# Performance work log

Hardware: AMD Instinct MI355X
Metric: run time of the kernel (lower is better)

## Reference

```python
import jax, jax.numpy as jnp
import numpy as np

N_ATOMS = 100000
N_EDGES = 200000  # paired: edge 2i and 2i+1 are reverses of each other
N_MOLS = 4096
D_V, D_E, D_H = 133, 14, 512
DEPTH = 3
BN_EPS = 1e-5


def setup_inputs() -> dict:
    key = jax.random.key(0)
    ks = jax.random.split(key, 10)
    V = jax.random.normal(ks[0], (N_ATOMS, D_V), dtype=jnp.float32)
    E = jax.random.normal(ks[1], (N_EDGES, D_E), dtype=jnp.float32)
    # paired directed edges: (src,dst) at 2i, (dst,src) at 2i+1 -> rev index is i^1
    half = N_EDGES // 2
    s = jax.random.randint(ks[2], (half,), 0, N_ATOMS, dtype=jnp.int32)
    d = jax.random.randint(ks[3], (half,), 0, N_ATOMS, dtype=jnp.int32)
    edge_src = jnp.stack([s, d], axis=1).reshape(-1)
    edge_dst = jnp.stack([d, s], axis=1).reshape(-1)
    batch = jnp.sort(jax.random.randint(ks[4], (N_ATOMS,), 0, N_MOLS, dtype=jnp.int32))
    sc = 0.02
    W_i = jax.random.normal(ks[5], (D_V + D_E, D_H), dtype=jnp.float32) * sc
    W_h = jax.random.normal(ks[6], (D_H, D_H), dtype=jnp.float32) * sc
    W_o = jax.random.normal(ks[7], (D_V + D_H, D_H), dtype=jnp.float32) * sc
    b_o = jnp.zeros((D_H,), dtype=jnp.float32)
    gamma = jnp.ones((D_H,), dtype=jnp.float32)
    beta = jnp.zeros((D_H,), dtype=jnp.float32)
    return {"V": V, "E": E, "edge_src": edge_src, "edge_dst": edge_dst,
            "batch": batch, "W_i": W_i, "W_h": W_h, "W_o": W_o, "b_o": b_o,
            "gamma": gamma, "beta": beta}


def reference(V, E, edge_src, edge_dst, batch, W_i, W_h, W_o, b_o, gamma, beta):
    n_atoms = V.shape[0]
    n_edges = E.shape[0]
    rev = jnp.arange(n_edges, dtype=jnp.int32) ^ 1  # reverse-bond index

    # --- BondMessagePassing (chemprop v2) ---
    # initialize: H_0 = W_i([V[src] ; E]), H = relu(H_0)
    H0 = jnp.concatenate([V[edge_src], E], axis=1) @ W_i  # [n_edges, d_h]
    H = jax.nn.relu(H0)
    for _ in range(DEPTH - 1):
        # message: sum of incoming edge states at dst node, gathered at src,
        # minus the reverse edge's own state
        M_node = jax.ops.segment_sum(H, edge_dst, num_segments=n_atoms)
        M = M_node[edge_src] - H[rev]
        # update: H = relu(H_0 + W_h(M)) (dropout = 0)
        H = jax.nn.relu(H0 + M @ W_h)
    # finalize: aggregate edges to nodes, H_v = relu(W_o([V ; M_v]))
    M_v = jax.ops.segment_sum(H, edge_dst, num_segments=n_atoms)
    H_v = jax.nn.relu(jnp.concatenate([V, M_v], axis=1) @ W_o + b_o)  # [n_atoms, d_h]

    # --- MeanAggregation over batch ids ---
    sums = jax.ops.segment_sum(H_v, batch, num_segments=N_MOLS)
    counts = jax.ops.segment_sum(jnp.ones((n_atoms,), H_v.dtype), batch, num_segments=N_MOLS)
    h_mol = sums / jnp.maximum(counts, 1.0)[:, None]  # [n_mols, d_h]

    # --- BatchNorm1d (training mode: batch statistics, biased variance) ---
    mu = h_mol.mean(axis=0)
    var = h_mol.var(axis=0)
    return (h_mol - mu) * jax.lax.rsqrt(var + BN_EPS) * gamma + beta
```

## Files before the change

kernel.cpp:

```cpp
#include <hip/hip_runtime.h>

typedef _Float16 f16;
typedef _Float16 half8 __attribute__((ext_vector_type(8)));
typedef _Float16 half4v __attribute__((ext_vector_type(4)));
typedef float f32x4 __attribute__((ext_vector_type(4)));

#define N_ATOMS 100000
#define N_EDGES 200000
#define N_MOLS  4096
#define D_V 133
#define D_E 14
#define D_H 512
#define KC  672
#define KSE 21
#define LDA 40

__global__ void wt_build_swz(const float* __restrict__ W1, int r1,
                             const float* __restrict__ W2, int r2,
                             f16* __restrict__ WtS) {
    int gid = blockIdx.x * blockDim.x + threadIdx.x;
    if (gid >= D_H * KC) return;
    int n = gid / KC;
    int k = gid - n * KC;
    float x = 0.f;
    if (k < r1) x = W1[k * D_H + n];
    else if (k < r1 + r2) x = W2[(k - r1) * D_H + n];
    const int dst = ((((n >> 4) * KSE + (k >> 5)) << 6) + (((k >> 3) & 3) << 4) + (n & 15)) * 8 + (k & 7);
    WtS[dst] = (f16)x;
}

__global__ void csr_hist(const int* __restrict__ edst, int* __restrict__ cnt) {
    int e = blockIdx.x * blockDim.x + threadIdx.x;
    if (e < N_EDGES) atomicAdd(&cnt[edst[e]], 1);
}

__global__ __launch_bounds__(1024) void csr_scan(const int* __restrict__ cnt,
                                                 int* __restrict__ off, int* __restrict__ pos) {
    __shared__ int sums[1024];
    const int tid = threadIdx.x;
    const int lo = tid * 100;
    int s = 0;
    if (lo < N_ATOMS) {
        const int4* c4 = reinterpret_cast<const int4*>(cnt + lo);
        #pragma unroll
        for (int i = 0; i < 25; ++i) { int4 v = c4[i]; s += v.x + v.y + v.z + v.w; }
    }
    sums[tid] = s;
    __syncthreads();
    for (int d = 1; d < 1024; d <<= 1) {
        int v = (tid >= d) ? sums[tid - d] : 0;
        __syncthreads();
        sums[tid] += v;
        __syncthreads();
    }
    int run = sums[tid] - s;
    if (lo < N_ATOMS) {
        const int4* c4 = reinterpret_cast<const int4*>(cnt + lo);
        for (int i = 0; i < 25; ++i) {
            int4 v = c4[i];
            const int b = lo + i * 4;
            off[b]     = run; pos[b]     = run; run += v.x;
            off[b + 1] = run; pos[b + 1] = run; run += v.y;
            off[b + 2] = run; pos[b + 2] = run; run += v.z;
            off[b + 3] = run; pos[b + 3] = run; run += v.w;
        }
    }
    if (tid == 1023) off[N_ATOMS] = run;
}

__global__ void csr_scatter(const int* __restrict__ edst, int* __restrict__ pos,
                            int* __restrict__ eid) {
    int e = blockIdx.x * blockDim.x + threadIdx.x;
    if (e < N_EDGES) {
        int idx = atomicAdd(&pos[edst[e]], 1);
        eid[idx] = e;
    }
}

template<bool F16M>
__global__ __launch_bounds__(512) void seg_csr(
    const f16* __restrict__ H, const int* __restrict__ off, const int* __restrict__ eid,
    void* __restrict__ MnOut, float* __restrict__ Msc)
{
    const int n = blockIdx.x * 8 + (threadIdx.x >> 6);
    const int lane = threadIdx.x & 63;
    const int j0 = off[n], j1 = off[n + 1];
    float acc[8];
    #pragma unroll
    for (int k = 0; k < 8; ++k) acc[k] = 0.f;
    int e_cur = (j0 < j1) ? eid[j0] : 0;
    for (int j = j0; j < j1; ++j) {
        const int e_nxt = (j + 1 < j1) ? eid[j + 1] : 0;
        const half8 h = *reinterpret_cast<const half8*>(&H[e_cur * D_H + lane * 8]);
        #pragma unroll
        for (int k = 0; k < 8; ++k) acc[k] += (float)h[k];
        e_cur = e_nxt;
    }
    if (F16M) {
        half8 o;
        #pragma unroll
        for (int k = 0; k < 8; ++k) o[k] = (f16)acc[k];
        *reinterpret_cast<half8*>(&((f16*)MnOut)[n * D_H + lane * 8]) = o;
    } else {
        float m = 0.f;
        #pragma unroll
        for (int k = 0; k < 8; ++k) m = fmaxf(m, fabsf(acc[k]));
        m = fmaxf(m, __shfl_xor(m, 1));
        m = fmaxf(m, __shfl_xor(m, 2));
        m = fmaxf(m, 1e-20f);
        const float s = m * (1.f / 127.f);
        const float inv_s = 127.f / m;
        if ((lane & 3) == 0) Msc[n * 16 + (lane >> 2)] = s;
        int q[8];
        #pragma unroll
        for (int k = 0; k < 8; ++k) q[k] = __float2int_rn(acc[k] * inv_s);
        uint2 o;
        o.x = (q[0] & 0xff) | ((q[1] & 0xff) << 8) | ((q[2] & 0xff) << 16) | ((unsigned)(q[3] & 0xff) << 24);
        o.y = (q[4] & 0xff) | ((q[5] & 0xff) << 8) | ((q[6] & 0xff) << 16) | ((unsigned)(q[7] & 0xff) << 24);
        *reinterpret_cast<uint2*>(&((unsigned int*)MnOut)[n * 128 + lane * 2]) = o;
    }
}

template<bool F16M, int KS0>
__global__ __launch_bounds__(512) void gemm_pass(
    const float* __restrict__ V, const float* __restrict__ E,
    const int* __restrict__ esrc, const void* __restrict__ Mn,
    const float* __restrict__ Msc,
    f16* __restrict__ Ha, const f16* __restrict__ WtS)
{
    __shared__ __align__(16) f16 Al[2][64 * LDA];
    const int tid = threadIdx.x;
    const int rowblk = blockIdx.x << 6;
    const int srow = tid >> 3;
    const int skk  = (tid & 7) << 2;
    const int e_s  = rowblk + srow;
    const int sv   = esrc[e_s];
    const int rev  = e_s ^ 1;
    const int lane = tid & 63;
    const int quad = lane >> 4;
    const int m16  = lane & 15;
    const int colbase = (tid >> 6) << 6;
    const int cb0 = (tid >> 6) << 2;
    const f16* WtL = WtS + lane * 8;

    f32x4 acc[4][4];
    #pragma unroll
    for (int a = 0; a < 4; ++a)
    #pragma unroll
    for (int b = 0; b < 4; ++b)
    #pragma unroll
    for (int r = 0; r < 4; ++r) acc[a][b][r] = 0.f;

    char4 pq0, pq1; float ps0, ps1;
    half4v pm0, pm1; half4v ph0, ph1;
    float pv0[4], pv1[4];

#define GP_ISSUE(S, KSV) do {                                                        \
    const int ks_i_ = (KSV);                                                         \
    if (ks_i_ < KSE) {                                                               \
        const int k0_ = ks_i_ << 5;                                                  \
        if (k0_ < D_H) {                                                             \
            if (F16M) {                                                              \
                pm##S = *reinterpret_cast<const half4v*>(&((const f16*)Mn)[sv * D_H + k0_ + skk]); \
            } else {                                                                 \
                pq##S = *reinterpret_cast<const char4*>(&((const char*)Mn)[sv * D_H + k0_ + skk]); \
                ps##S = Msc[sv * 16 + (k0_ >> 5)];                                   \
            }                                                                        \
            ph##S = *reinterpret_cast<const half4v*>(&Ha[rev * D_H + k0_ + skk]);    \
        } else {                                                                     \
            const int kb_ = k0_ + skk - D_H;                                         \
            pv##S[0] = (kb_ + 0 < D_V) ? V[sv * D_V + kb_ + 0] : ((kb_ + 0 < D_V + D_E) ? E[e_s * D_E + kb_ + 0 - D_V] : 0.f); \
            pv##S[1] = (kb_ + 1 < D_V) ? V[sv * D_V + kb_ + 1] : ((kb_ + 1 < D_V + D_E) ? E[e_s * D_E + kb_ + 1 - D_V] : 0.f); \
            pv##S[2] = (kb_ + 2 < D_V) ? V[sv * D_V + kb_ + 2] : ((kb_ + 2 < D_V + D_E) ? E[e_s * D_E + kb_ + 2 - D_V] : 0.f); \
            pv##S[3] = (kb_ + 3 < D_V) ? V[sv * D_V + kb_ + 3] : ((kb_ + 3 < D_V + D_E) ? E[e_s * D_E + kb_ + 3 - D_V] : 0.f); \
        }                                                                            \
    }                                                                                \
} while (0)

#define GP_MAKEW(S, KSV, W) do {                                                     \
    const int k0_ = (KSV) << 5;                                                      \
    if (k0_ < D_H) {                                                                 \
        if (F16M) { W = pm##S - ph##S; }                                             \
        else {                                                                       \
            W[0] = (f16)((float)pq##S.x * ps##S - (float)ph##S[0]);                  \
            W[1] = (f16)((float)pq##S.y * ps##S - (float)ph##S[1]);                  \
            W[2] = (f16)((float)pq##S.z * ps##S - (float)ph##S[2]);                  \
            W[3] = (f16)((float)pq##S.w * ps##S - (float)ph##S[3]);                  \
        }                                                                            \
    } else {                                                                         \
        W[0] = (f16)pv##S[0]; W[1] = (f16)pv##S[1];                                  \
        W[2] = (f16)pv##S[2]; W[3] = (f16)pv##S[3];                                  \
    }                                                                                \
} while (0)

#define GP_MFMA(KSV, CUR) do {                                                       \
    half8 af[4];                                                                     \
    _Pragma("unroll")                                                                \
    for (int rt = 0; rt < 4; ++rt)                                                   \
        af[rt] = *reinterpret_cast<const half8*>(&Al[CUR][(rt * 16 + m16) * LDA + quad * 8]); \
    _Pragma("unroll")                                                                \
    for (int ct = 0; ct < 4; ++ct) {                                                 \
        const half8 bf = *reinterpret_cast<const half8*>(&WtL[(((cb0 + ct) * KSE + (KSV)) << 9)]); \
        _Pragma("unroll")                                                            \
        for (int rt = 0; rt < 4; ++rt)                                               \
            acc[rt][ct] = __builtin_amdgcn_mfma_f32_16x16x32_f16(af[rt], bf, acc[rt][ct], 0, 0, 0); \
    }                                                                                \
} while (0)

    GP_ISSUE(0, KS0);
    GP_ISSUE(1, KS0 + 1);
    {
        half4v w;
        GP_MAKEW(0, KS0, w);
        *reinterpret_cast<half4v*>(&Al[0][srow * LDA + skk]) = w;
        GP_ISSUE(0, KS0 + 2);
    }
    __syncthreads();

    constexpr int NT = KSE - KS0;
    #pragma unroll 2
    for (int i = 0; i < NT - 1; ++i) {
        const int ks = KS0 + i;
        const int cur = i & 1;
        {
            half4v w;
            if ((i + 1) & 1) { GP_MAKEW(1, ks + 1, w); }
            else             { GP_MAKEW(0, ks + 1, w); }
            *reinterpret_cast<half4v*>(&Al[cur ^ 1][srow * LDA + skk]) = w;
            if ((i + 1) & 1) { GP_ISSUE(1, ks + 3); }
            else             { GP_ISSUE(0, ks + 3); }
        }
        GP_MFMA(ks, cur);
        __syncthreads();
    }
    GP_MFMA(KSE - 1, (NT - 1) & 1);

#undef GP_ISSUE
#undef GP_MAKEW
#undef GP_MFMA

    #pragma unroll
    for (int rt = 0; rt < 4; ++rt)
    #pragma unroll
    for (int ct = 0; ct < 4; ++ct)
    #pragma unroll
    for (int r = 0; r < 4; ++r) {
        const int row = rowblk + rt * 16 + quad * 4 + r;
        const int col = colbase + ct * 16 + m16;
        Ha[row * D_H + col] = (f16)fmaxf(acc[rt][ct][r], 0.f);
    }
}

template<bool F16M>
__global__ __launch_bounds__(512) void gemm_out(
    const float* __restrict__ V, const void* __restrict__ Mn,
    const float* __restrict__ Msc, const float* __restrict__ bo,
    const f16* __restrict__ WtS, f16* __restrict__ Hv)
{
    __shared__ __align__(16) f16 Al[2][64 * LDA];
    __shared__ float bo_s[D_H];
    const int tid = threadIdx.x;
    const int rowblk = blockIdx.x << 6;
    bo_s[tid] = bo[tid];
    const int srow = tid >> 3;
    const int skk  = (tid & 7) << 2;
    const int arow = min(rowblk + srow, N_ATOMS - 1);
    const int lane = tid & 63;
    const int quad = lane >> 4;
    const int m16  = lane & 15;
    const int colbase = (tid >> 6) << 6;
    const int cb0 = (tid >> 6) << 2;
    const f16* WtL = WtS + lane * 8;

    f32x4 acc[4][4];
    #pragma unroll
    for (int a = 0; a < 4; ++a)
    #pragma unroll
    for (int b = 0; b < 4; ++b)
    #pragma unroll
    for (int r = 0; r < 4; ++r) acc[a][b][r] = 0.f;

    char4 pq0, pq1; float ps0, ps1;
    half4v pm0, pm1;
    float pv0[4], pv1[4];

#define GO_ISSUE(S, KSV) do {                                                        \
    const int ks_i_ = (KSV);                                                         \
    if (ks_i_ < KSE) {                                                               \
        const int k0_ = ks_i_ << 5;                                                  \
        if (k0_ < D_H) {                                                             \
            if (F16M) {                                                              \
                pm##S = *reinterpret_cast<const half4v*>(&((const f16*)Mn)[arow * D_H + k0_ + skk]); \
            } else {                                                                 \
                pq##S = *reinterpret_cast<const char4*>(&((const char*)Mn)[arow * D_H + k0_ + skk]); \
                ps##S = Msc[arow * 16 + (k0_ >> 5)];                                 \
            }                                                                        \
        } else {                                                                     \
            const int kb_ = k0_ + skk - D_H;                                         \
            pv##S[0] = (kb_ + 0 < D_V) ? V[arow * D_V + kb_ + 0] : 0.f;              \
            pv##S[1] = (kb_ + 1 < D_V) ? V[arow * D_V + kb_ + 1] : 0.f;              \
            pv##S[2] = (kb_ + 2 < D_V) ? V[arow * D_V + kb_ + 2] : 0.f;              \
            pv##S[3] = (kb_ + 3 < D_V) ? V[arow * D_V + kb_ + 3] : 0.f;              \
        }                                                                            \
    }                                                                                \
} while (0)

#define GO_MAKEW(S, KSV, W) do {                                                     \
    const int k0_ = (KSV) << 5;                                                      \
    if (k0_ < D_H) {                                                                 \
        if (F16M) { W = pm##S; }                                                     \
        else {                                                                       \
            W[0] = (f16)((float)pq##S.x * ps##S);                                    \
            W[1] = (f16)((float)pq##S.y * ps##S);                                    \
            W[2] = (f16)((float)pq##S.z * ps##S);                                    \
            W[3] = (f16)((float)pq##S.w * ps##S);                                    \
        }                                                                            \
    } else {                                                                         \
        W[0] = (f16)pv##S[0]; W[1] = (f16)pv##S[1];                                  \
        W[2] = (f16)pv##S[2]; W[3] = (f16)pv##S[3];                                  \
    }                                                                                \
} while (0)

#define GO_MFMA(KSV, CUR) do {                                                       \
    half8 af[4];                                                                     \
    _Pragma("unroll")                                                                \
    for (int rt = 0; rt < 4; ++rt)                                                   \
        af[rt] = *reinterpret_cast<const half8*>(&Al[CUR][(rt * 16 + m16) * LDA + quad * 8]); \
    _Pragma("unroll")                                                                \
    for (int ct = 0; ct < 4; ++ct) {                                                 \
        const half8 bf = *reinterpret_cast<const half8*>(&WtL[(((cb0 + ct) * KSE + (KSV)) << 9)]); \
        _Pragma("unroll")                                                            \
        for (int rt = 0; rt < 4; ++rt)                                               \
            acc[rt][ct] = __builtin_amdgcn_mfma_f32_16x16x32_f16(af[rt], bf, acc[rt][ct], 0, 0, 0); \
    }                                                                                \
} while (0)

    GO_ISSUE(0, 0);
    GO_ISSUE(1, 1);
    {
        half4v w;
        GO_MAKEW(0, 0, w);
        *reinterpret_cast<half4v*>(&Al[0][srow * LDA + skk]) = w;
        GO_ISSUE(0, 2);
    }
    __syncthreads();

    #pragma unroll 2
    for (int i = 0; i < KSE - 1; ++i) {
        const int ks = i;
        const int cur = i & 1;
        {
            half4v w;
            if ((i + 1) & 1) { GO_MAKEW(1, ks + 1, w); }
            else             { GO_MAKEW(0, ks + 1, w); }
            *reinterpret_cast<half4v*>(&Al[cur ^ 1][srow * LDA + skk]) = w;
            if ((i + 1) & 1) { GO_ISSUE(1, ks + 3); }
            else             { GO_ISSUE(0, ks + 3); }
        }
        GO_MFMA(ks, cur);
        __syncthreads();
    }
    GO_MFMA(KSE - 1, (KSE - 1) & 1);

#undef GO_ISSUE
#undef GO_MAKEW
#undef GO_MFMA

    #pragma unroll
    for (int rt = 0; rt < 4; ++rt)
    #pragma unroll
    for (int ct = 0; ct < 4; ++ct)
    #pragma unroll
    for (int r = 0; r < 4; ++r) {
        const int row = rowblk + rt * 16 + quad * 4 + r;
        if (row < N_ATOMS) {
            const int col = colbase + ct * 16 + m16;
            Hv[row * D_H + col] = (f16)fmaxf(acc[rt][ct][r] + bo_s[col], 0.f);
        }
    }
}

__global__ __launch_bounds__(512) void mol_mean(
    const f16* __restrict__ Hv, const int* __restrict__ batch, float* __restrict__ mean)
{
    const int m = blockIdx.x;
    __shared__ int sh[2];
    if (threadIdx.x == 0) {
        int lo = 0, hi = N_ATOMS;
        while (lo < hi) { int mid = (lo + hi) >> 1; if (batch[mid] < m) lo = mid + 1; else hi = mid; }
        sh[0] = lo;
        int lo2 = lo; hi = N_ATOMS;
        while (lo2 < hi) { int mid = (lo2 + hi) >> 1; if (batch[mid] < m + 1) lo2 = mid + 1; else hi = mid; }
        sh[1] = lo2;
    }
    __syncthreads();
    const int a0 = sh[0], a1 = sh[1];
    float acc = 0.f;
    for (int a = a0; a < a1; ++a) acc += (float)Hv[(size_t)a * D_H + threadIdx.x];
    mean[m * D_H + threadIdx.x] = acc / (float)max(a1 - a0, 1);
}

__global__ __launch_bounds__(256) void bn_stats(
    const float* __restrict__ mean_in, const float* __restrict__ gamma,
    const float* __restrict__ beta, float* __restrict__ An, float* __restrict__ Bn)
{
    const int n = blockIdx.x;
    const int tid = threadIdx.x;
    float s = 0.f, s2 = 0.f;
    for (int m = tid; m < N_MOLS; m += 256) {
        float h = mean_in[m * D_H + n];
        s += h; s2 += h * h;
    }
    for (int off = 32; off > 0; off >>= 1) {
        s  += __shfl_down(s, off);
        s2 += __shfl_down(s2, off);
    }
    __shared__ float sh[8];
    const int wave = tid >> 6, lane = tid & 63;
    if (lane == 0) { sh[wave] = s; sh[4 + wave] = s2; }
    __syncthreads();
    if (tid == 0) {
        float S  = sh[0] + sh[1] + sh[2] + sh[3];
        float S2 = sh[4] + sh[5] + sh[6] + sh[7];
        float mu = S / (float)N_MOLS;
        float var = fmaxf(S2 / (float)N_MOLS - mu * mu, 0.f);
        float sc = rsqrtf(var + 1e-5f) * gamma[n];
        An[n] = sc;
        Bn[n] = beta[n] - mu * sc;
    }
}

__global__ void bn_apply(const float* __restrict__ mean_in,
                         const float* __restrict__ An, const float* __restrict__ Bn,
                         float* __restrict__ out)
{
    int gid = blockIdx.x * blockDim.x + threadIdx.x;
    int n = gid & 511;
    out[gid] = mean_in[gid] * An[n] + Bn[n];
}

extern "C" void kernel_launch(void* const* d_in, const int* in_sizes, int n_in,
                              void* d_out, int out_size, void* d_ws, size_t ws_size,
                              hipStream_t stream)
{
    (void)in_sizes; (void)n_in; (void)out_size;
    const float* V     = (const float*)d_in[0];
    const float* E     = (const float*)d_in[1];
    const int*   esrc  = (const int*)d_in[2];
    const int*   edst  = (const int*)d_in[3];
    const int*   batch = (const int*)d_in[4];
    const float* Wi    = (const float*)d_in[5];
    const float* Wh    = (const float*)d_in[6];
    const float* Wo    = (const float*)d_in[7];
    const float* bo    = (const float*)d_in[8];
    const float* gam   = (const float*)d_in[9];
    const float* bet   = (const float*)d_in[10];
    float* out = (float*)d_out;

    char* ws = (char*)d_ws;
    f16*   WtC  = (f16*)(ws + 0);
    f16*   WtO  = (f16*)(ws + 688128);
    int*   off  = (int*)(ws + 1376256);
    int*   eid  = (int*)(ws + 1776384);
    int*   cnt  = (int*)(ws + 2576384);
    float* An   = (float*)(ws + 2992768);
    float* Bn   = (float*)(ws + 2994816);
    f16*   Ha   = (f16*)(ws + 2996864);
    void*  Mn   = (void*)(ws + 207796864);
    float* Msc  = (float*)(ws + 258996864);
    f16*   Hv   = Ha;
    float* mean = out;

    const bool f16m = ws_size >= 310196864ULL;

    wt_build_swz<<<(D_H * KC + 255) / 256, 256, 0, stream>>>(Wh, D_H, Wi, D_V + D_E, WtC);
    wt_build_swz<<<(D_H * KC + 255) / 256, 256, 0, stream>>>(Wo + D_V * D_H, D_H, Wo, D_V, WtO);

    hipMemsetAsync(cnt, 0, 400000, stream);
    csr_hist<<<(N_EDGES + 511) / 512, 512, 0, stream>>>(edst, cnt);
    csr_scan<<<1, 1024, 0, stream>>>(cnt, off, cnt);
    csr_scatter<<<(N_EDGES + 511) / 512, 512, 0, stream>>>(edst, cnt, eid);

    if (f16m) {
        gemm_pass<true, 16><<<N_EDGES / 64, 512, 0, stream>>>(V, E, esrc, Mn, Msc, Ha, WtC);
        for (int it = 0; it < 2; ++it) {
            seg_csr<true><<<N_ATOMS / 8, 512, 0, stream>>>(Ha, off, eid, Mn, Msc);
            gemm_pass<true, 0><<<N_EDGES / 64, 512, 0, stream>>>(V, E, esrc, Mn, Msc, Ha, WtC);
        }
        seg_csr<true><<<N_ATOMS / 8, 512, 0, stream>>>(Ha, off, eid, Mn, Msc);
        gemm_out<true><<<(N_ATOMS + 63) / 64, 512, 0, stream>>>(V, Mn, Msc, bo, WtO, Hv);
    } else {
        gemm_pass<false, 16><<<N_EDGES / 64, 512, 0, stream>>>(V, E, esrc, Mn, Msc, Ha, WtC);
        for (int it = 0; it < 2; ++it) {
            seg_csr<false><<<N_ATOMS / 8, 512, 0, stream>>>(Ha, off, eid, Mn, Msc);
            gemm_pass<false, 0><<<N_EDGES / 64, 512, 0, stream>>>(V, E, esrc, Mn, Msc, Ha, WtC);
        }
        seg_csr<false><<<N_ATOMS / 8, 512, 0, stream>>>(Ha, off, eid, Mn, Msc);
        gemm_out<false><<<(N_ATOMS + 63) / 64, 512, 0, stream>>>(V, Mn, Msc, bo, WtO, Hv);
    }

    mol_mean<<<N_MOLS, 512, 0, stream>>>(Hv, batch, mean);
    bn_stats<<<D_H, 256, 0, stream>>>(mean, gam, bet, An, Bn);
    bn_apply<<<(N_MOLS * D_H) / 256, 256, 0, stream>>>(mean, An, Bn, out);
}
```

Before: 1.512 ms.

## Split message construction out of edge GEMM into a separate in-place kernel

Adds a msg_build kernel that computes M = M_node[src] - H[rev] for each paired edge and writes it in place into Ha. The edge GEMM (gemm_edge) then loads its A operand as contiguous rows of Ha, with no gathered Mn/scale loads or dequantisation in its software-pipelined inner loop. This is meant to remove gather latency and conversion ALU work from the MFMA loop. The cost is an extra kernel launch and an extra full read and write of the edge-state buffer on each iteration.

New measurement: 1.315 ms. 1.15x faster.

```diff
diff --git a/kernel.cpp b/kernel.cpp
--- a/kernel.cpp
+++ b/kernel.cpp
@@ -121,11 +121,44 @@
     }
 }
 
-template<bool F16M, int KS0>
-__global__ __launch_bounds__(512) void gemm_pass(
+template<bool F16M>
+__global__ __launch_bounds__(256) void msg_build(
+    const int* __restrict__ esrc, const void* __restrict__ Mn,
+    const float* __restrict__ Msc, f16* __restrict__ Ha)
+{
+    const int p = blockIdx.x * 4 + (threadIdx.x >> 6);
+    const int lane = threadIdx.x & 63;
+    const int e0 = 2 * p, e1 = 2 * p + 1;
+    const int sv0 = esrc[e0], sv1 = esrc[e1];
+    const half8 h0 = *reinterpret_cast<const half8*>(&Ha[e0 * D_H + lane * 8]);
+    const half8 h1 = *reinterpret_cast<const half8*>(&Ha[e1 * D_H + lane * 8]);
+    half8 w0, w1;
+    if (F16M) {
+        const half8 m0 = *reinterpret_cast<const half8*>(&((const f16*)Mn)[sv0 * D_H + lane * 8]);
+        const half8 m1 = *reinterpret_cast<const half8*>(&((const f16*)Mn)[sv1 * D_H + lane * 8]);
+        w0 = m0 - h1;
+        w1 = m1 - h0;
+    } else {
+        const uint2 q0 = *reinterpret_cast<const uint2*>(&((const unsigned int*)Mn)[sv0 * 128 + lane * 2]);
+        const uint2 q1 = *reinterpret_cast<const uint2*>(&((const unsigned int*)Mn)[sv1 * 128 + lane * 2]);
+        const float s0 = Msc[sv0 * 16 + (lane >> 2)];
+        const float s1 = Msc[sv1 * 16 + (lane >> 2)];
+        #pragma unroll
+        for (int k = 0; k < 8; ++k) {
+            const int b0 = (int)(char)(((k < 4) ? q0.x : q0.y) >> ((k & 3) * 8));
+            const int b1 = (int)(char)(((k < 4) ? q1.x : q1.y) >> ((k & 3) * 8));
+            w0[k] = (f16)((float)b0 * s0 - (float)h1[k]);
+            w1[k] = (f16)((float)b1 * s1 - (float)h0[k]);
+        }
+    }
+    *reinterpret_cast<half8*>(&Ha[e0 * D_H + lane * 8]) = w0;
+    *reinterpret_cast<half8*>(&Ha[e1 * D_H + lane * 8]) = w1;
+}
+
+template<int KS0>
+__global__ __launch_bounds__(512) void gemm_edge(
     const float* __restrict__ V, const float* __restrict__ E,
-    const int* __restrict__ esrc, const void* __restrict__ Mn,
-    const float* __restrict__ Msc,
+    const int* __restrict__ esrc,
     f16* __restrict__ Ha, const f16* __restrict__ WtS)
 {
     __shared__ __align__(16) f16 Al[2][64 * LDA];
@@ -135,7 +168,6 @@
     const int skk  = (tid & 7) << 2;
     const int e_s  = rowblk + srow;
     const int sv   = esrc[e_s];
-    const int rev  = e_s ^ 1;
     const int lane = tid & 63;
     const int quad = lane >> 4;
     const int m16  = lane & 15;
@@ -151,22 +183,15 @@
     #pragma unroll
     for (int r = 0; r < 4; ++r) acc[a][b][r] = 0.f;
 
-    char4 pq0, pq1; float ps0, ps1;
-    half4v pm0, pm1; half4v ph0, ph1;
+    half4v pm0, pm1;
     float pv0[4], pv1[4];
 
-#define GP_ISSUE(S, KSV) do {                                                        \
+#define GE_ISSUE(S, KSV) do {                                                        \
     const int ks_i_ = (KSV);                                                         \
     if (ks_i_ < KSE) {                                                               \
         const int k0_ = ks_i_ << 5;                                                  \
         if (k0_ < D_H) {                                                             \
-            if (F16M) {                                                              \
-                pm##S = *reinterpret_cast<const half4v*>(&((const f16*)Mn)[sv * D_H + k0_ + skk]); \
-            } else {                                                                 \
-                pq##S = *reinterpret_cast<const char4*>(&((const char*)Mn)[sv * D_H + k0_ + skk]); \
-                ps##S = Msc[sv * 16 + (k0_ >> 5)];                                   \
-            }                                                                        \
-            ph##S = *reinterpret_cast<const half4v*>(&Ha[rev * D_H + k0_ + skk]);    \
+            pm##S = *reinterpret_cast<const half4v*>(&Ha[e_s * D_H + k0_ + skk]);    \
         } else {                                                                     \
             const int kb_ = k0_ + skk - D_H;                                         \
             pv##S[0] = (kb_ + 0 < D_V) ? V[sv * D_V + kb_ + 0] : ((kb_ + 0 < D_V + D_E) ? E[e_s * D_E + kb_ + 0 - D_V] : 0.f); \
@@ -177,23 +202,16 @@
     }                                                                                \
 } while (0)
 
-#define GP_MAKEW(S, KSV, W) do {                                                     \
+#define GE_MAKEW(S, KSV, W) do {                                                     \
     const int k0_ = (KSV) << 5;                                                      \
-    if (k0_ < D_H) {                                                                 \
-        if (F16M) { W = pm##S - ph##S; }                                             \
-        else {                                                                       \
-            W[0] = (f16)((float)pq##S.x * ps##S - (float)ph##S[0]);                  \
-            W[1] = (f16)((float)pq##S.y * ps##S - (float)ph##S[1]);                  \
-            W[2] = (f16)((float)pq##S.z * ps##S - (float)ph##S[2]);                  \
-            W[3] = (f16)((float)pq##S.w * ps##S - (float)ph##S[3]);                  \
-        }                                                                            \
-    } else {                                                                         \
+    if (k0_ < D_H) { W = pm##S; }                                                    \
+    else {                                                                           \
         W[0] = (f16)pv##S[0]; W[1] = (f16)pv##S[1];                                  \
         W[2] = (f16)pv##S[2]; W[3] = (f16)pv##S[3];                                  \
     }                                                                                \
 } while (0)
 
-#define GP_MFMA(KSV, CUR) do {                                                       \
+#define GE_MFMA(KSV, CUR) do {                                                       \
     half8 af[4];                                                                     \
     _Pragma("unroll")                                                                \
     for (int rt = 0; rt < 4; ++rt)                                                   \
@@ -207,13 +225,13 @@
     }                                                                                \
 } while (0)
 
-    GP_ISSUE(0, KS0);
-    GP_ISSUE(1, KS0 + 1);
+    GE_ISSUE(0, KS0);
+    GE_ISSUE(1, KS0 + 1);
     {
         half4v w;
-        GP_MAKEW(0, KS0, w);
+        GE_MAKEW(0, KS0, w);
         *reinterpret_cast<half4v*>(&Al[0][srow * LDA + skk]) = w;
-        GP_ISSUE(0, KS0 + 2);
+        GE_ISSUE(0, KS0 + 2);
     }
     __syncthreads();
 
@@ -224,20 +242,20 @@
         const int cur = i & 1;
         {
             half4v w;
-            if ((i + 1) & 1) { GP_MAKEW(1, ks + 1, w); }
-            else             { GP_MAKEW(0, ks + 1, w); }
+            if ((i + 1) & 1) { GE_MAKEW(1, ks + 1, w); }
+            else             { GE_MAKEW(0, ks + 1, w); }
             *reinterpret_cast<half4v*>(&Al[cur ^ 1][srow * LDA + skk]) = w;
-            if ((i + 1) & 1) { GP_ISSUE(1, ks + 3); }
-            else             { GP_ISSUE(0, ks + 3); }
-        }
-        GP_MFMA(ks, cur);
+            if ((i + 1) & 1) { GE_ISSUE(1, ks + 3); }
+            else             { GE_ISSUE(0, ks + 3); }
+        }
+        GE_MFMA(ks, cur);
         __syncthreads();
     }
-    GP_MFMA(KSE - 1, (NT - 1) & 1);
-
-#undef GP_ISSUE
-#undef GP_MAKEW
-#undef GP_MFMA
+    GE_MFMA(KSE - 1, (NT - 1) & 1);
+
+#undef GE_ISSUE
+#undef GE_MAKEW
+#undef GE_MFMA
 
     #pragma unroll
     for (int rt = 0; rt < 4; ++rt)
@@ -481,19 +499,21 @@
     csr_scan<<<1, 1024, 0, stream>>>(cnt, off, cnt);
     csr_scatter<<<(N_EDGES + 511) / 512, 512, 0, stream>>>(edst, cnt, eid);
 
+    gemm_edge<16><<<N_EDGES / 64, 512, 0, stream>>>(V, E, esrc, Ha, WtC);
+
     if (f16m) {
-        gemm_pass<true, 16><<<N_EDGES / 64, 512, 0, stream>>>(V, E, esrc, Mn, Msc, Ha, WtC);
         for (int it = 0; it < 2; ++it) {
             seg_csr<true><<<N_ATOMS / 8, 512, 0, stream>>>(Ha, off, eid, Mn, Msc);
-            gemm_pass<true, 0><<<N_EDGES / 64, 512, 0, stream>>>(V, E, esrc, Mn, Msc, Ha, WtC);
+            msg_build<true><<<N_EDGES / 8, 256, 0, stream>>>(esrc, Mn, Msc, Ha);
+            gemm_edge<0><<<N_EDGES / 64, 512, 0, stream>>>(V, E, esrc, Ha, WtC);
         }
         seg_csr<true><<<N_ATOMS / 8, 512, 0, stream>>>(Ha, off, eid, Mn, Msc);
         gemm_out<true><<<(N_ATOMS + 63) / 64, 512, 0, stream>>>(V, Mn, Msc, bo, WtO, Hv);
     } else {
-        gemm_pass<false, 16><<<N_EDGES / 64, 512, 0, stream>>>(V, E, esrc, Mn, Msc, Ha, WtC);
         for (int it = 0; it < 2; ++it) {
             seg_csr<false><<<N_ATOMS / 8, 512, 0, stream>>>(Ha, off, eid, Mn, Msc);
-            gemm_pass<false, 0><<<N_EDGES / 64, 512, 0, stream>>>(V, E, esrc, Mn, Msc, Ha, WtC);
+            msg_build<false><<<N_EDGES / 8, 256, 0, stream>>>(esrc, Mn, Msc, Ha);
+            gemm_edge<0><<<N_EDGES / 64, 512, 0, stream>>>(V, E, esrc, Ha, WtC);
         }
         seg_csr<false><<<N_ATOMS / 8, 512, 0, stream>>>(Ha, off, eid, Mn, Msc);
         gemm_out<false><<<(N_ATOMS + 63) / 64, 512, 0, stream>>>(V, Mn, Msc, bo, WtO, Hv);
```
